# Performance work log

Measured on AMD Instinct MI355X. Metric: run time of the kernel, lower is better.

The kernel has to match this reference:

```python
import jax, jax.numpy as jnp
import numpy as np

DEPTH = 4
DIM = 128
M_DIM = 16
FEAT_DIM = 10
K = 12
CLAMP = 2.0
B, N = 4, 2048
EI = 2 * DIM + 1  # edge_input_dim = feats_i + feats_j + rel_dist


def setup_inputs() -> dict:
    key = jax.random.key(0)
    ks = jax.random.split(key, 16)
    def p(k, shape, s=0.05):
        return jax.random.normal(k, shape, dtype=jnp.float32) * s
    inp = dict(
        feats=jax.random.normal(ks[0], (B, N, FEAT_DIM), dtype=jnp.float32),
        coords=jax.random.normal(ks[1], (B, N, 3), dtype=jnp.float32) * 3.0,
        mask=jnp.ones((B, N), dtype=bool),
        emb_w=p(ks[2], (FEAT_DIM, DIM)), emb_b=p(ks[3], (DIM,)),
        ew1=p(ks[4], (DEPTH, EI, 2 * EI)), eb1=p(ks[5], (DEPTH, 2 * EI)),
        ew2=p(ks[6], (DEPTH, 2 * EI, M_DIM)), eb2=p(ks[7], (DEPTH, M_DIM)),
        cw1=p(ks[8], (DEPTH, M_DIM, 4 * M_DIM)), cb1=p(ks[9], (DEPTH, 4 * M_DIM)),
        cw2=p(ks[10], (DEPTH, 4 * M_DIM, 1)), cb2=p(ks[11], (DEPTH, 1)),
        cscale=jnp.full((DEPTH, 1), 1e-2, dtype=jnp.float32),  # CoorsNorm scale_init
        nw1=p(ks[12], (DEPTH, DIM + M_DIM, 2 * DIM)), nb1=p(ks[13], (DEPTH, 2 * DIM)),
        nw2=p(ks[14], (DEPTH, 2 * DIM, DIM)), nb2=p(ks[15], (DEPTH, DIM)),
    )
    return inp


def _egnn_layer(feats, coors, mask, lp):
    ew1, eb1, ew2, eb2, cw1, cb1, cw2, cb2, cscale, nw1, nb1, nw2, nb2 = lp
    # pairwise relative coords / squared distances
    rel = coors[:, :, None, :] - coors[:, None, :, :]            # (B,N,N,3)
    dist = jnp.sum(rel * rel, axis=-1)                           # (B,N,N)
    pm = mask[:, :, None] & mask[:, None, :]
    ranking = jnp.where(pm, dist, 1e5)
    _, nbhd = jax.lax.top_k(-ranking, K)                         # (B,N,K) smallest dists
    rel_k = jnp.take_along_axis(rel, nbhd[..., None], axis=2)    # (B,N,K,3)
    dist_k = jnp.take_along_axis(dist, nbhd, axis=2)             # (B,N,K)
    feats_j = jax.vmap(lambda f, i: f[i])(feats, nbhd)           # (B,N,K,D)
    mask_j = jnp.take_along_axis(jnp.broadcast_to(mask[:, None, :], dist.shape), nbhd, axis=2)
    m2 = mask[:, :, None] & mask_j                               # (B,N,K)
    feats_i = jnp.broadcast_to(feats[:, :, None, :], feats_j.shape)
    edge_in = jnp.concatenate([feats_i, feats_j, dist_k[..., None]], axis=-1)  # (B,N,K,EI)
    m_ij = jax.nn.silu(jax.nn.silu(edge_in @ ew1 + eb1) @ ew2 + eb2)           # (B,N,K,M)
    # coordinate update (E(n)-equivariant)
    w = (jax.nn.silu(m_ij @ cw1 + cb1) @ cw2 + cb2)[..., 0]      # (B,N,K)
    nrm = jnp.sqrt(jnp.sum(rel_k * rel_k, axis=-1, keepdims=True))
    rel_n = rel_k / jnp.maximum(nrm, 1e-8) * cscale              # CoorsNorm
    w = jnp.clip(jnp.where(m2, w, 0.0), -CLAMP, CLAMP)
    coors_out = coors + jnp.einsum('bik,bikc->bic', w, rel_n)
    # node update (residual)
    m_i = jnp.sum(jnp.where(m2[..., None], m_ij, 0.0), axis=2)   # (B,N,M)
    node_in = jnp.concatenate([feats, m_i], axis=-1)
    feats_out = jax.nn.silu(node_in @ nw1 + nb1) @ nw2 + nb2 + feats
    return feats_out, coors_out


def reference(feats, coords, mask, emb_w, emb_b, ew1, eb1, ew2, eb2, cw1, cb1, cw2, cb2, cscale, nw1, nb1, nw2, nb2):
    h = feats @ emb_w + emb_b                                    # continuous feature embedding
    c = coords
    for l in range(DEPTH):
        lp = (ew1[l], eb1[l], ew2[l], eb2[l], cw1[l], cb1[l], cw2[l], cb2[l],
              cscale[l], nw1[l], nb1[l], nw2[l], nb2[l])
        h, c = _egnn_layer(h, c, mask, lp)
    mf = mask.astype(h.dtype)
    out = jnp.sum(h * mf[..., None], axis=1) / jnp.sum(mf, axis=1, keepdims=True)  # (B,DIM)
    return out
```

## Files before the change

### kernel.cpp

```cpp
#include <hip/hip_runtime.h>
#include <hip/hip_bf16.h>
#include <math.h>

#define NB 4
#define NN 2048
#define DIMF 128
#define MD 16
#define KK 12
#define NODES (NB*NN)

typedef __attribute__((ext_vector_type(8))) short bf16x8;
typedef __attribute__((ext_vector_type(4))) float f32x4;

__device__ __forceinline__ float silu_f(float x) {
    return x * __builtin_amdgcn_rcpf(1.0f + __expf(-x));
}

__device__ __forceinline__ short f2bf(float x) {
    unsigned u = __float_as_uint(x);
    unsigned r = (u + 0x7FFFu + ((u >> 16) & 1u)) >> 16;
    return (short)r;
}

__device__ __forceinline__ short2 pkbf(float a, float b) {
    union { __hip_bfloat162 h; short2 s; } u;
    u.h = __float22bfloat162_rn(make_float2(a, b));
    return u.s;
}

__device__ __forceinline__ void upk8(uint4 u, float* f) {
    f[0] = __uint_as_float(u.x << 16); f[1] = __uint_as_float(u.x & 0xFFFF0000u);
    f[2] = __uint_as_float(u.y << 16); f[3] = __uint_as_float(u.y & 0xFFFF0000u);
    f[4] = __uint_as_float(u.z << 16); f[5] = __uint_as_float(u.z & 0xFFFF0000u);
    f[6] = __uint_as_float(u.w << 16); f[7] = __uint_as_float(u.w & 0xFFFF0000u);
}

__device__ __forceinline__ void knn_body(const float* __restrict__ coords,
                                         int* __restrict__ nbhd,
                                         int b2, int tid, float* sc) {
    int batch = b2 >> 9;
    int qbase = (b2 & 511) << 2;
    const float* cb = coords + (size_t)batch * NN * 3;
    const float4* cb4 = (const float4*)cb;
    int wv = tid >> 6, lane = tid & 63;
    int ql = qbase + wv;
    float qx = cb[3 * ql], qy = cb[3 * ql + 1], qz = cb[3 * ql + 2];
    float kd[KK]; int ki[KK];
#pragma unroll
    for (int r = 0; r < KK; ++r) { kd[r] = 3.0e38f; ki[r] = -1; }
#pragma unroll
    for (int half = 0; half < 2; ++half) {
#pragma unroll
        for (int t = 0; t < 3; ++t) {
            int e = tid + t * 256;
            ((float4*)sc)[e] = cb4[half * 768 + e];
        }
        __syncthreads();
#pragma unroll 4
        for (int jj = 0; jj < 16; ++jj) {
            int jl = (jj << 6) + lane;
            float dx = sc[3 * jl] - qx, dy = sc[3 * jl + 1] - qy, dz = sc[3 * jl + 2] - qz;
            float d2 = dx * dx + dy * dy + dz * dz;
            float cv = d2; int cix = (half << 10) + jl;
#pragma unroll
            for (int r = 0; r < KK; ++r) {
                bool sw = cv < kd[r];
                float tv = sw ? kd[r] : cv; int ti = sw ? ki[r] : cix;
                kd[r] = sw ? cv : kd[r];    ki[r] = sw ? cix : ki[r];
                cv = tv; cix = ti;
            }
        }
        __syncthreads();
    }
    int* out = nbhd + ((size_t)batch * NN + ql) * KK;
#pragma unroll
    for (int pass = 0; pass < KK; ++pass) {
        float mv = kd[0]; int mj = ki[0];
#pragma unroll
        for (int o = 1; o < 64; o <<= 1) {
            float ov = __shfl_xor(mv, o);
            int   oj = __shfl_xor(mj, o);
            if (ov < mv || (ov == mv && oj < mj)) { mv = ov; mj = oj; }
        }
        if (lane == 0) out[pass] = batch * NN + mj;
        if (kd[0] == mv && ki[0] == mj) {
#pragma unroll
            for (int r = 0; r < KK - 1; ++r) { kd[r] = kd[r + 1]; ki[r] = ki[r + 1]; }
            kd[KK - 1] = 3.0e38f;
        }
    }
}

template<typename AT, typename OT, int ACT, int RPW>
__device__ __forceinline__ void mgemm_body(
    const AT* __restrict__ A, int lda,
    const float* __restrict__ Bm, int ldb,
    OT* __restrict__ C, int ldc,
    const float* __restrict__ bias,
    const float* __restrict__ resid, int ldr,
    int N, int K, int bx, int by, int tid,
    unsigned short (*sA)[40], unsigned short (*sBt)[40])
{
    constexpr bool AF32 = (sizeof(AT) == 4);
    int lane = tid & 63, w = tid >> 6, quad = lane >> 4, l16 = lane & 15;
    int rowBase = by * (RPW * 64);
    int colBase = bx * 64;
    f32x4 acc[RPW][4];
#pragma unroll
    for (int rt = 0; rt < RPW; ++rt)
#pragma unroll
        for (int ct = 0; ct < 4; ++ct) acc[rt][ct] = (f32x4){0.f, 0.f, 0.f, 0.f};

    int kend = (K + 31) >> 5;
    for (int kc = 0; kc < kend; ++kc) {
        int k0 = kc * 32;
        if constexpr (AF32) {
#pragma unroll
            for (int p = 0; p < RPW * 2; ++p) {
                int e = tid + p * 256;
                int r = e >> 3, kq = e & 7, kg = k0 + kq * 4;
                short4 sv = {0, 0, 0, 0};
                if (kg + 4 <= K) {
                    float4 v = *(const float4*)&A[(size_t)(rowBase + r) * lda + kg];
                    short2 a = pkbf(v.x, v.y), b = pkbf(v.z, v.w);
                    sv = make_short4(a.x, a.y, b.x, b.y);
                }
                *(short4*)&sA[r][kq * 4] = sv;
            }
        } else {
#pragma unroll
            for (int p = 0; p < RPW; ++p) {
                int e = tid + p * 256;
                int r = e >> 2, k8 = (e & 3) * 8, kg = k0 + k8;
                uint4 v = {0u, 0u, 0u, 0u};
                if (kg + 8 <= K)
                    v = *(const uint4*)&A[(size_t)(rowBase + r) * lda + kg];
                *(uint4*)&sA[r][k8] = v;
            }
        }
#pragma unroll
        for (int p = 0; p < 4; ++p) {
            int e = tid + p * 256;
            int kk = e >> 5, c2 = (e & 31) * 2, kg = k0 + kk;
            int c0 = colBase + c2;
            float v0 = (kg < K && c0 < N)     ? Bm[(size_t)kg * ldb + c0]     : 0.0f;
            float v1 = (kg < K && c0 + 1 < N) ? Bm[(size_t)kg * ldb + c0 + 1] : 0.0f;
            sBt[c2][kk]     = (unsigned short)f2bf(v0);
            sBt[c2 + 1][kk] = (unsigned short)f2bf(v1);
        }
        __syncthreads();
        bf16x8 a[RPW], b[4];
#pragma unroll
        for (int rt = 0; rt < RPW; ++rt)
            a[rt] = *(const bf16x8*)&sA[w * (RPW * 16) + rt * 16 + l16][quad * 8];
#pragma unroll
        for (int ct = 0; ct < 4; ++ct)
            b[ct] = *(const bf16x8*)&sBt[ct * 16 + l16][quad * 8];
#pragma unroll
        for (int rt = 0; rt < RPW; ++rt)
#pragma unroll
            for (int ct = 0; ct < 4; ++ct)
                acc[rt][ct] = __builtin_amdgcn_mfma_f32_16x16x32_bf16(a[rt], b[ct], acc[rt][ct], 0, 0, 0);
        __syncthreads();
    }
#pragma unroll
    for (int rt = 0; rt < RPW; ++rt) {
#pragma unroll
        for (int ct = 0; ct < 4; ++ct) {
            int col = colBase + ct * 16 + l16;
            if (col < N) {
                float bv = bias ? bias[col] : 0.0f;
#pragma unroll
                for (int r = 0; r < 4; ++r) {
                    int row = rowBase + w * (RPW * 16) + rt * 16 + quad * 4 + r;
                    float v = acc[rt][ct][r] + bv;
                    if (ACT) v = silu_f(v);
                    if (resid) v += resid[(size_t)row * ldr + col];
                    if constexpr (sizeof(OT) == 4)
                        C[(size_t)row * ldc + col] = v;
                    else
                        C[(size_t)row * ldc + col] = (OT)f2bf(v);
                }
            }
        }
    }
}

template<typename AT, typename OT, int ACT, int RPW>
__global__ __launch_bounds__(256) void mgemm_kernel(
    const AT* __restrict__ A, int lda,
    const float* __restrict__ Bm, int ldb,
    OT* __restrict__ C, int ldc,
    const float* __restrict__ bias,
    const float* __restrict__ resid, int ldr,
    int N, int K)
{
    __shared__ __attribute__((aligned(16))) unsigned short sA[RPW * 64][40];
    __shared__ __attribute__((aligned(16))) unsigned short sBt[64][40];
    mgemm_body<AT, OT, ACT, RPW>(A, lda, Bm, ldb, C, ldc, bias, resid, ldr,
                                 N, K, blockIdx.x, blockIdx.y, threadIdx.x, sA, sBt);
}

__global__ __launch_bounds__(256) void embed_knn_kernel(
    const float* __restrict__ feats, const float* __restrict__ w,
    const float* __restrict__ b, float* __restrict__ h,
    const float* __restrict__ coords, int* __restrict__ nbhd)
{
    __shared__ __attribute__((aligned(16))) float sc[3072];
    int tid = threadIdx.x;
    if ((int)blockIdx.x < 2048) {
        knn_body(coords, nbhd, blockIdx.x, tid, sc);
    } else {
        int idx = ((int)blockIdx.x - 2048) * 256 + tid;
        int n = idx >> 7, d = idx & 127;
        const float* fr = feats + n * 10;
        float acc = b[d];
#pragma unroll
        for (int f = 0; f < 10; ++f) acc = fmaf(fr[f], w[f * 128 + d], acc);
        h[idx] = acc;
    }
}

__global__ __launch_bounds__(256) void mlp1knn_kernel(
    const float* __restrict__ nodein_, const float* __restrict__ nw1l,
    unsigned short* __restrict__ t1b, const float* __restrict__ nb1l,
    const float* __restrict__ coordsN, int* __restrict__ nbhd, int knnb)
{
    __shared__ __attribute__((aligned(16))) char smem[15360];
    int tid = threadIdx.x;
    if ((int)blockIdx.x < knnb) {
        knn_body(coordsN, nbhd, blockIdx.x, tid, (float*)smem);
    } else {
        int q = (int)blockIdx.x - knnb;
        mgemm_body<float, unsigned short, 1, 1>(
            nodein_, 144, nw1l, 256, t1b, 256, nb1l, nullptr, 0,
            256, 144, q & 3, q >> 2, tid,
            (unsigned short(*)[40])smem, (unsigned short(*)[40])(smem + 5120));
    }
}

__global__ __launch_bounds__(256) void pq_gemm_kernel(
    const float* __restrict__ A,
    const float* __restrict__ B1, const float* __restrict__ B2,
    unsigned short* __restrict__ PQb,
    const float* __restrict__ bias)
{
    __shared__ __attribute__((aligned(16))) unsigned short sA[128][40];
    __shared__ __attribute__((aligned(16))) unsigned short sBt[64][40];
    int tid = threadIdx.x;
    int lane = tid & 63, w = tid >> 6, quad = lane >> 4, l16 = lane & 15;
    int rowBase = blockIdx.y * 128;
    int colBase = blockIdx.x * 64;
    f32x4 acc[2][4];
#pragma unroll
    for (int rt = 0; rt < 2; ++rt)
#pragma unroll
        for (int ct = 0; ct < 4; ++ct) acc[rt][ct] = (f32x4){0.f, 0.f, 0.f, 0.f};

#pragma unroll
    for (int kc = 0; kc < 4; ++kc) {
        int k0 = kc * 32;
#pragma unroll
        for (int p = 0; p < 4; ++p) {
            int e = tid + p * 256;
            int r = e >> 3, kq = e & 7;
            float4 v = *(const float4*)&A[(size_t)(rowBase + r) * 128 + k0 + kq * 4];
            short2 a = pkbf(v.x, v.y), b = pkbf(v.z, v.w);
            *(short4*)&sA[r][kq * 4] = make_short4(a.x, a.y, b.x, b.y);
        }
#pragma unroll
        for (int p = 0; p < 4; ++p) {
            int e = tid + p * 256;
            int kk = e >> 5, c2 = (e & 31) * 2, kg = k0 + kk;
            int c0 = colBase + c2;
            float v0 = 0.0f, v1 = 0.0f;
            if (c0 < 1028) {
                const float* Bp = (c0 < 514) ? B1 : B2;
                int cc = (c0 < 514) ? c0 : c0 - 514;
                v0 = Bp[(size_t)kg * 514 + cc];
            }
            if (c0 + 1 < 1028) {
                const float* Bp = (c0 + 1 < 514) ? B1 : B2;
                int cc = (c0 + 1 < 514) ? c0 + 1 : c0 + 1 - 514;
                v1 = Bp[(size_t)kg * 514 + cc];
            }
            sBt[c2][kk]     = (unsigned short)f2bf(v0);
            sBt[c2 + 1][kk] = (unsigned short)f2bf(v1);
        }
        __syncthreads();
        bf16x8 a[2], b[4];
#pragma unroll
        for (int rt = 0; rt < 2; ++rt)
            a[rt] = *(const bf16x8*)&sA[w * 32 + rt * 16 + l16][quad * 8];
#pragma unroll
        for (int ct = 0; ct < 4; ++ct)
            b[ct] = *(const bf16x8*)&sBt[ct * 16 + l16][quad * 8];
#pragma unroll
        for (int rt = 0; rt < 2; ++rt)
#pragma unroll
            for (int ct = 0; ct < 4; ++ct)
                acc[rt][ct] = __builtin_amdgcn_mfma_f32_16x16x32_bf16(a[rt], b[ct], acc[rt][ct], 0, 0, 0);
        __syncthreads();
    }
#pragma unroll
    for (int rt = 0; rt < 2; ++rt) {
#pragma unroll
        for (int ct = 0; ct < 4; ++ct) {
            int col = colBase + ct * 16 + l16;
            if (col < 1028) {
                bool isP = col < 514;
                int oc = isP ? col : col + 14;
                float bv = isP ? bias[col] : 0.0f;
#pragma unroll
                for (int r = 0; r < 4; ++r) {
                    int row = rowBase + w * 32 + rt * 16 + quad * 4 + r;
                    PQb[(size_t)row * 1056 + oc] = (unsigned short)f2bf(acc[rt][ct][r] + bv);
                }
            }
        }
    }
}

__global__ __launch_bounds__(192, 6) void edge_kernel(
    const unsigned short* __restrict__ PQ, const int* __restrict__ nbhd,
    const float* __restrict__ cin, float* __restrict__ cout,
    float* __restrict__ nodein, const float* __restrict__ hin,
    const float* __restrict__ wrow,
    const float* __restrict__ ew2l,
    const float* __restrict__ cw1l,
    const float* __restrict__ eb2l,
    const float* __restrict__ cb1l,
    const float* __restrict__ cw2l,
    const float* __restrict__ cb2l,
    const float* __restrict__ cscalel)
{
    __shared__ __attribute__((aligned(16))) unsigned short sB[17][64][8];
    __shared__ __attribute__((aligned(16))) float swl[544];
    int tid = threadIdx.x;

    for (int idx = tid; idx < 8704; idx += 192) {
        int kc = idx >> 9, ln = (idx >> 3) & 63, j = idx & 7;
        int k = kc * 32 + ((ln >> 4) << 3) + j, n = ln & 15;
        sB[kc][ln][j] = (k < 514) ? (unsigned short)f2bf(ew2l[k * 16 + n]) : (unsigned short)0;
    }
    for (int idx = tid; idx < 544; idx += 192)
        swl[idx] = (idx < 514) ? wrow[idx] : 0.0f;
    __syncthreads();

    int lane = tid & 63, w = tid >> 6;
    int quad = lane >> 4, e16 = lane & 15;
    int eloc = w * 16 + e16;
    int nloc = eloc / 12;
    int k12 = eloc - nloc * 12;
    int bid = blockIdx.x;
    int rr8 = bid & 7, bsw = rr8 >> 1;
    int wsw = ((bid >> 3) << 1) | (rr8 & 1);
    int nodeBase = bsw * 2048 + wsw * 4;
    int i = nodeBase + nloc;
    int j = nbhd[i * KK + k12];
    float cix = cin[i * 3], ciy = cin[i * 3 + 1], ciz = cin[i * 3 + 2];
    float rx = cix - cin[j * 3], ry = ciy - cin[j * 3 + 1], rz = ciz - cin[j * 3 + 2];
    float d2 = rx * rx + ry * ry + rz * rz;

    const unsigned short* Pp = PQ + (size_t)i * 1056 + quad * 8;
    const unsigned short* Qp = PQ + (size_t)j * 1056 + 528 + quad * 8;

    uint4 pb[3], qb[3];
    pb[0] = *(const uint4*)Pp;
    qb[0] = *(const uint4*)Qp;
    pb[1] = *(const uint4*)(Pp + 32);
    qb[1] = *(const uint4*)(Qp + 32);

    f32x4 acc = {0.0f, 0.0f, 0.0f, 0.0f};
#pragma unroll
    for (int kc = 0; kc < 16; ++kc) {
        int cur = kc % 3, nx = (kc + 2) % 3;
        if (kc < 14) {
            pb[nx] = *(const uint4*)(Pp + (kc + 2) * 32);
            qb[nx] = *(const uint4*)(Qp + (kc + 2) * 32);
        }
        float p[8], q[8];
        upk8(pb[cur], p); upk8(qb[cur], q);
        float4 w0 = *(const float4*)&swl[quad * 8 + kc * 32];
        float4 w1 = *(const float4*)&swl[quad * 8 + kc * 32 + 4];
        float h0 = silu_f(fmaf(d2, w0.x, p[0] + q[0]));
        float h1 = silu_f(fmaf(d2, w0.y, p[1] + q[1]));
        float h2 = silu_f(fmaf(d2, w0.z, p[2] + q[2]));
        float h3 = silu_f(fmaf(d2, w0.w, p[3] + q[3]));
        float h4 = silu_f(fmaf(d2, w1.x, p[4] + q[4]));
        float h5 = silu_f(fmaf(d2, w1.y, p[5] + q[5]));
        float h6 = silu_f(fmaf(d2, w1.z, p[6] + q[6]));
        float h7 = silu_f(fmaf(d2, w1.w, p[7] + q[7]));
        bf16x8 af;
        short2 r0 = pkbf(h0, h1), r1 = pkbf(h2, h3), r2 = pkbf(h4, h5), r3 = pkbf(h6, h7);
        af[0] = r0.x; af[1] = r0.y; af[2] = r1.x; af[3] = r1.y;
        af[4] = r2.x; af[5] = r2.y; af[6] = r3.x; af[7] = r3.y;
        bf16x8 bf = *(const bf16x8*)&sB[kc][lane][0];
        acc = __builtin_amdgcn_mfma_f32_16x16x32_bf16(af, bf, acc, 0, 0, 0);
    }
    {
        unsigned up = *(const unsigned*)(PQ + (size_t)i * 1056 + 512);
        unsigned uq = *(const unsigned*)(PQ + (size_t)j * 1056 + 528 + 512);
        bf16x8 af = {0, 0, 0, 0, 0, 0, 0, 0};
        if (quad == 0) {
            float px = __uint_as_float(up << 16), py = __uint_as_float(up & 0xFFFF0000u);
            float qx = __uint_as_float(uq << 16), qy = __uint_as_float(uq & 0xFFFF0000u);
            af[0] = f2bf(silu_f(fmaf(d2, swl[512], px + qx)));
            af[1] = f2bf(silu_f(fmaf(d2, swl[513], py + qy)));
        }
        bf16x8 bf = *(const bf16x8*)&sB[16][lane][0];
        acc = __builtin_amdgcn_mfma_f32_16x16x32_bf16(af, bf, acc, 0, 0, 0);
    }

    float eb = eb2l[e16];
    float m[4];
#pragma unroll
    for (int r = 0; r < 4; ++r) m[r] = silu_f(acc[r] + eb);

    __syncthreads();
    unsigned short* sCp = (unsigned short*)sB;
    unsigned short* mbf = (unsigned short*)((char*)sB + 4096);
    float* mf32         = (float*)((char*)sB + 5632);
    float* reld2        = (float*)((char*)sB + 8704);
    float* wall         = (float*)((char*)sB + 9472);
    for (int idx = tid; idx < 2048; idx += 192) {
        int nb = idx >> 9, ln = (idx >> 3) & 63, jj = idx & 7;
        int c = ((ln >> 4) << 3) + jj, n = nb * 16 + (ln & 15);
        sCp[idx] = (c < 16) ? (unsigned short)f2bf(cw1l[c * 64 + n]) : (unsigned short)0;
    }
#pragma unroll
    for (int r = 0; r < 4; ++r) {
        int row = w * 16 + quad * 4 + r;
        mbf[row * 16 + e16] = (unsigned short)f2bf(m[r]);
        mf32[row * 16 + e16] = m[r];
    }
    if (quad == 0) {
        int eo = (w * 16 + e16) * 4;
        reld2[eo] = rx; reld2[eo + 1] = ry; reld2[eo + 2] = rz; reld2[eo + 3] = d2;
    }
    __syncthreads();

    if (tid < 64) {
        int n = tid >> 4, ch = tid & 15;
        float s = 0.0f;
#pragma unroll
        for (int ke = 0; ke < KK; ++ke) s += mf32[(n * 12 + ke) * 16 + ch];
        nodein[(size_t)(nodeBase + n) * 144 + 128 + ch] = s;
    }

    bf16x8 af2 = {0, 0, 0, 0, 0, 0, 0, 0};
    if (quad < 2) af2 = *(const bf16x8*)&mbf[(w * 16 + e16) * 16 + quad * 8];
    float wpart[4] = {0.0f, 0.0f, 0.0f, 0.0f};
#pragma unroll
    for (int nb = 0; nb < 4; ++nb) {
        bf16x8 cf = *(const bf16x8*)(sCp + ((nb * 64 + lane) << 3));
        f32x4 z = {0.0f, 0.0f, 0.0f, 0.0f};
        f32x4 t = __builtin_amdgcn_mfma_f32_16x16x32_bf16(af2, cf, z, 0, 0, 0);
        int d = nb * 16 + e16;
        float cb = cb1l[d], cw = cw2l[d];
#pragma unroll
        for (int r = 0; r < 4; ++r)
            wpart[r] = fmaf(silu_f(t[r] + cb), cw, wpart[r]);
    }
#pragma unroll
    for (int o = 1; o < 16; o <<= 1)
#pragma unroll
        for (int r = 0; r < 4; ++r) wpart[r] += __shfl_xor(wpart[r], o);
    if (e16 == 0) {
        float cb2v = cb2l[0];
#pragma unroll
        for (int r = 0; r < 4; ++r) {
            float ww = wpart[r] + cb2v;
            ww = fminf(fmaxf(ww, -2.0f), 2.0f);
            wall[w * 16 + quad * 4 + r] = ww;
        }
    }
    __syncthreads();

    if (tid < 12) {
        int n = tid / 3, c = tid - n * 3;
        float cs = cscalel[0];
        float s = 0.0f;
#pragma unroll
        for (int ke = 0; ke < KK; ++ke) {
            int eo = (n * 12 + ke) * 4;
            float d2e = reld2[eo + 3];
            float f = wall[n * 12 + ke] * cs * __builtin_amdgcn_rcpf(fmaxf(sqrtf(d2e), 1e-8f));
            s = fmaf(f, reld2[eo + c], s);
        }
        int node = nodeBase + n;
        cout[node * 3 + c] = cin[node * 3 + c] + s;
    }

    if (tid < 128) {
        int rr = tid >> 5, c4 = (tid & 31) * 4;
        *(float4*)&nodein[(size_t)(nodeBase + rr) * 144 + c4] =
            *(const float4*)&hin[(size_t)(nodeBase + rr) * 128 + c4];
    }
}

__global__ __launch_bounds__(256) void final1_kernel(const float* __restrict__ h,
                                                     float* __restrict__ part) {
    int b = blockIdx.x >> 5, sl = blockIdx.x & 31;
    int d = threadIdx.x & 127, half = threadIdx.x >> 7;
    const float* hp = h + ((size_t)b * NN + sl * 64) * DIMF;
    float acc = 0.0f;
    for (int n = half; n < 64; n += 2) acc += hp[(size_t)n * DIMF + d];
    __shared__ float red[256];
    red[threadIdx.x] = acc;
    __syncthreads();
    if (half == 0) part[(size_t)blockIdx.x * DIMF + d] = red[d] + red[d + 128];
}

__global__ __launch_bounds__(128) void final2_kernel(const float* __restrict__ part,
                                                     float* __restrict__ out) {
    int b = blockIdx.x, d = threadIdx.x;
    float acc = 0.0f;
#pragma unroll
    for (int s = 0; s < 32; ++s) acc += part[(size_t)(b * 32 + s) * DIMF + d];
    out[b * DIMF + d] = acc * (1.0f / NN);
}

extern "C" void kernel_launch(void* const* d_in, const int* in_sizes, int n_in,
                              void* d_out, int out_size, void* d_ws, size_t ws_size,
                              hipStream_t stream) {
    const float* feats  = (const float*)d_in[0];
    const float* coords = (const float*)d_in[1];
    const float* emb_w  = (const float*)d_in[3];
    const float* emb_b  = (const float*)d_in[4];
    const float* ew1    = (const float*)d_in[5];
    const float* eb1    = (const float*)d_in[6];
    const float* ew2    = (const float*)d_in[7];
    const float* eb2    = (const float*)d_in[8];
    const float* cw1    = (const float*)d_in[9];
    const float* cb1    = (const float*)d_in[10];
    const float* cw2    = (const float*)d_in[11];
    const float* cb2    = (const float*)d_in[12];
    const float* cscale = (const float*)d_in[13];
    const float* nw1    = (const float*)d_in[14];
    const float* nb1    = (const float*)d_in[15];
    const float* nw2    = (const float*)d_in[16];
    const float* nb2    = (const float*)d_in[17];

    char* ws = (char*)d_ws;
    float* h0     = (float*)(ws + 0);
    float* h1     = (float*)(ws + 4194304);
    float* c0     = (float*)(ws + 8388608);
    float* c1     = (float*)(ws + 8486912);
    int*   nbhd   = (int*)  (ws + 8585216);
    float* nodein = (float*)(ws + 8978432);
    unsigned short* PQb = (unsigned short*)(ws + 13697024);
    unsigned short* t1b = (unsigned short*)(ws + 31457280);
    float* part   = (float*)(ws + 13697024);

    float* hbuf[2] = {h0, h1};
    float* cbuf[2] = {c0, c1};

    embed_knn_kernel<<<6144, 256, 0, stream>>>(feats, emb_w, emb_b, h0, coords, nbhd);

    for (int l = 0; l < 4; ++l) {
        const float* hin  = hbuf[l & 1];
        float*       hout = hbuf[(l + 1) & 1];
        const float* cin  = (l == 0) ? coords : cbuf[(l - 1) & 1];
        float*       cout = cbuf[l & 1];
        const float* ew1l = ew1 + (size_t)l * 257 * 514;

        pq_gemm_kernel<<<dim3(17, 64), 256, 0, stream>>>(
            hin, ew1l, ew1l + 128 * 514, PQb, eb1 + l * 514);

        edge_kernel<<<NODES / 4, 192, 0, stream>>>(PQb, nbhd, cin, cout, nodein, hin,
            ew1l + 256 * 514, ew2 + (size_t)l * 514 * 16, cw1 + (size_t)l * 1024,
            eb2 + l * 16, cb1 + l * 64, cw2 + l * 64, cb2 + l, cscale + l);

        int knnb = (l < 3) ? 2048 : 0;
        mlp1knn_kernel<<<knnb + 512, 256, 0, stream>>>(
            nodein, nw1 + (size_t)l * 144 * 256, t1b, nb1 + l * 256,
            cout, nbhd, knnb);

        mgemm_kernel<unsigned short, float, 0, 1><<<dim3(2, 128), 256, 0, stream>>>(
            t1b, 256, nw2 + (size_t)l * 256 * 128, 128, hout, 128,
            nb2 + l * 128, hin, 128, 128, 256);
    }

    final1_kernel<<<NB * 32, 256, 0, stream>>>(hbuf[0], part);
    final2_kernel<<<NB, 128, 0, stream>>>(part, (float*)d_out);
}
```

Baseline: 595.3 us.

## Pre-pack edge MLP weights into bf16 MFMA fragments and read them from global

Adds a one-time prep kernel that converts ew2 and cw1 for all layers into bf16 MFMA B-fragment layout in workspace. The edge kernel no longer stages these weights into shared memory each block, so it drops the per-block conversion loops, one barrier and most of the 17KB shared array, and it raises the occupancy hint from 6 to 8 blocks per SM. The weights are now fetched from global or cache inside the MFMA loop, which adds memory latency per iteration and relies on the small fragments staying cache-resident.

```diff
diff --git a/kernel.cpp b/kernel.cpp
--- a/kernel.cpp
+++ b/kernel.cpp
@@ -33,6 +33,27 @@
     f[2] = __uint_as_float(u.y << 16); f[3] = __uint_as_float(u.y & 0xFFFF0000u);
     f[4] = __uint_as_float(u.z << 16); f[5] = __uint_as_float(u.z & 0xFFFF0000u);
     f[6] = __uint_as_float(u.w << 16); f[7] = __uint_as_float(u.w & 0xFFFF0000u);
+}
+
+__global__ __launch_bounds__(256) void prep_kernel(const float* __restrict__ ew2,
+                                                   const float* __restrict__ cw1,
+                                                   unsigned short* __restrict__ ew2frag,
+                                                   unsigned short* __restrict__ cw1frag) {
+    int t = blockIdx.x * 256 + threadIdx.x;
+    if (t >= 43008) return;
+    int l = t / 10752, r = t % 10752;
+    if (r < 8704) {
+        int kc = r >> 9, lane = (r >> 3) & 63, j = r & 7;
+        int k = kc * 32 + ((lane >> 4) << 3) + j, n = lane & 15;
+        float v = (k < 514) ? ew2[(size_t)l * 514 * 16 + k * 16 + n] : 0.0f;
+        ew2frag[(size_t)l * 8704 + r] = (unsigned short)f2bf(v);
+    } else {
+        int r2 = r - 8704;
+        int nb = r2 >> 9, lane = (r2 >> 3) & 63, j = r2 & 7;
+        int c = ((lane >> 4) << 3) + j, n = nb * 16 + (lane & 15);
+        float v = (c < 16) ? cw1[(size_t)l * 1024 + c * 64 + n] : 0.0f;
+        cw1frag[(size_t)l * 2048 + r2] = (unsigned short)f2bf(v);
+    }
 }
 
 __device__ __forceinline__ void knn_body(const float* __restrict__ coords,
@@ -321,28 +342,26 @@
     }
 }
 
-__global__ __launch_bounds__(192, 6) void edge_kernel(
+__global__ __launch_bounds__(192, 8) void edge_kernel(
     const unsigned short* __restrict__ PQ, const int* __restrict__ nbhd,
     const float* __restrict__ cin, float* __restrict__ cout,
     float* __restrict__ nodein, const float* __restrict__ hin,
     const float* __restrict__ wrow,
-    const float* __restrict__ ew2l,
-    const float* __restrict__ cw1l,
+    const unsigned short* __restrict__ ew2f,
+    const unsigned short* __restrict__ cw1f,
     const float* __restrict__ eb2l,
     const float* __restrict__ cb1l,
     const float* __restrict__ cw2l,
     const float* __restrict__ cb2l,
     const float* __restrict__ cscalel)
 {
-    __shared__ __attribute__((aligned(16))) unsigned short sB[17][64][8];
     __shared__ __attribute__((aligned(16))) float swl[544];
+    __shared__ __attribute__((aligned(16))) unsigned short mbf[48][16];
+    __shared__ __attribute__((aligned(16))) float mf32[48][16];
+    __shared__ __attribute__((aligned(16))) float reld2[48][4];
+    __shared__ float wall[48];
     int tid = threadIdx.x;
 
-    for (int idx = tid; idx < 8704; idx += 192) {
-        int kc = idx >> 9, ln = (idx >> 3) & 63, j = idx & 7;
-        int k = kc * 32 + ((ln >> 4) << 3) + j, n = ln & 15;
-        sB[kc][ln][j] = (k < 514) ? (unsigned short)f2bf(ew2l[k * 16 + n]) : (unsigned short)0;
-    }
     for (int idx = tid; idx < 544; idx += 192)
         swl[idx] = (idx < 514) ? wrow[idx] : 0.0f;
     __syncthreads();
@@ -395,7 +414,7 @@
         short2 r0 = pkbf(h0, h1), r1 = pkbf(h2, h3), r2 = pkbf(h4, h5), r3 = pkbf(h6, h7);
         af[0] = r0.x; af[1] = r0.y; af[2] = r1.x; af[3] = r1.y;
         af[4] = r2.x; af[5] = r2.y; af[6] = r3.x; af[7] = r3.y;
-        bf16x8 bf = *(const bf16x8*)&sB[kc][lane][0];
+        bf16x8 bf = *(const bf16x8*)(ew2f + (((size_t)kc * 64 + lane) << 3));
         acc = __builtin_amdgcn_mfma_f32_16x16x32_bf16(af, bf, acc, 0, 0, 0);
     }
     {
@@ -408,7 +427,7 @@
             af[0] = f2bf(silu_f(fmaf(d2, swl[512], px + qx)));
             af[1] = f2bf(silu_f(fmaf(d2, swl[513], py + qy)));
         }
-        bf16x8 bf = *(const bf16x8*)&sB[16][lane][0];
+        bf16x8 bf = *(const bf16x8*)(ew2f + (((size_t)16 * 64 + lane) << 3));
         acc = __builtin_amdgcn_mfma_f32_16x16x32_bf16(af, bf, acc, 0, 0, 0);
     }
 
@@ -417,26 +436,15 @@
 #pragma unroll
     for (int r = 0; r < 4; ++r) m[r] = silu_f(acc[r] + eb);
 
-    __syncthreads();
-    unsigned short* sCp = (unsigned short*)sB;
-    unsigned short* mbf = (unsigned short*)((char*)sB + 4096);
-    float* mf32         = (float*)((char*)sB + 5632);
-    float* reld2        = (float*)((char*)sB + 8704);
-    float* wall         = (float*)((char*)sB + 9472);
-    for (int idx = tid; idx < 2048; idx += 192) {
-        int nb = idx >> 9, ln = (idx >> 3) & 63, jj = idx & 7;
-        int c = ((ln >> 4) << 3) + jj, n = nb * 16 + (ln & 15);
-        sCp[idx] = (c < 16) ? (unsigned short)f2bf(cw1l[c * 64 + n]) : (unsigned short)0;
-    }
 #pragma unroll
     for (int r = 0; r < 4; ++r) {
         int row = w * 16 + quad * 4 + r;
-        mbf[row * 16 + e16] = (unsigned short)f2bf(m[r]);
-        mf32[row * 16 + e16] = m[r];
+        mbf[row][e16] = (unsigned short)f2bf(m[r]);
+        mf32[row][e16] = m[r];
     }
     if (quad == 0) {
-        int eo = (w * 16 + e16) * 4;
-        reld2[eo] = rx; reld2[eo + 1] = ry; reld2[eo + 2] = rz; reld2[eo + 3] = d2;
+        reld2[eloc][0] = rx; reld2[eloc][1] = ry;
+        reld2[eloc][2] = rz; reld2[eloc][3] = d2;
     }
     __syncthreads();
 
@@ -444,16 +452,16 @@
         int n = tid >> 4, ch = tid & 15;
         float s = 0.0f;
 #pragma unroll
-        for (int ke = 0; ke < KK; ++ke) s += mf32[(n * 12 + ke) * 16 + ch];
+        for (int ke = 0; ke < KK; ++ke) s += mf32[n * 12 + ke][ch];
         nodein[(size_t)(nodeBase + n) * 144 + 128 + ch] = s;
     }
 
     bf16x8 af2 = {0, 0, 0, 0, 0, 0, 0, 0};
-    if (quad < 2) af2 = *(const bf16x8*)&mbf[(w * 16 + e16) * 16 + quad * 8];
+    if (quad < 2) af2 = *(const bf16x8*)&mbf[w * 16 + e16][quad * 8];
     float wpart[4] = {0.0f, 0.0f, 0.0f, 0.0f};
 #pragma unroll
     for (int nb = 0; nb < 4; ++nb) {
-        bf16x8 cf = *(const bf16x8*)(sCp + ((nb * 64 + lane) << 3));
+        bf16x8 cf = *(const bf16x8*)(cw1f + (((size_t)nb * 64 + lane) << 3));
         f32x4 z = {0.0f, 0.0f, 0.0f, 0.0f};
         f32x4 t = __builtin_amdgcn_mfma_f32_16x16x32_bf16(af2, cf, z, 0, 0, 0);
         int d = nb * 16 + e16;
@@ -483,10 +491,10 @@
         float s = 0.0f;
 #pragma unroll
         for (int ke = 0; ke < KK; ++ke) {
-            int eo = (n * 12 + ke) * 4;
-            float d2e = reld2[eo + 3];
-            float f = wall[n * 12 + ke] * cs * __builtin_amdgcn_rcpf(fmaxf(sqrtf(d2e), 1e-8f));
-            s = fmaf(f, reld2[eo + c], s);
+            int eo = n * 12 + ke;
+            float d2e = reld2[eo][3];
+            float f = wall[eo] * cs * __builtin_amdgcn_rcpf(fmaxf(sqrtf(d2e), 1e-8f));
+            s = fmaf(f, reld2[eo][c], s);
         }
         int node = nodeBase + n;
         cout[node * 3 + c] = cin[node * 3 + c] + s;
@@ -551,11 +559,14 @@
     float* nodein = (float*)(ws + 8978432);
     unsigned short* PQb = (unsigned short*)(ws + 13697024);
     unsigned short* t1b = (unsigned short*)(ws + 31457280);
+    unsigned short* ew2frag = (unsigned short*)(ws + 35651584);
+    unsigned short* cw1frag = (unsigned short*)(ws + 35721216);
     float* part   = (float*)(ws + 13697024);
 
     float* hbuf[2] = {h0, h1};
     float* cbuf[2] = {c0, c1};
 
+    prep_kernel<<<168, 256, 0, stream>>>(ew2, cw1, ew2frag, cw1frag);
     embed_knn_kernel<<<6144, 256, 0, stream>>>(feats, emb_w, emb_b, h0, coords, nbhd);
 
     for (int l = 0; l < 4; ++l) {
@@ -569,7 +580,7 @@
             hin, ew1l, ew1l + 128 * 514, PQb, eb1 + l * 514);
 
         edge_kernel<<<NODES / 4, 192, 0, stream>>>(PQb, nbhd, cin, cout, nodein, hin,
-            ew1l + 256 * 514, ew2 + (size_t)l * 514 * 16, cw1 + (size_t)l * 1024,
+            ew1l + 256 * 514, ew2frag + (size_t)l * 8704, cw1frag + (size_t)l * 2048,
             eb2 + l * 16, cb1 + l * 64, cw2 + l * 64, cb2 + l, cscale + l);
 
         int knnb = (l < 3) ? 2048 : 0;
```

Result: faster. 528.3 us (-11.3%).
